# Kernel optimization log

Hardware: AMD Instinct MI355X
Metric: run time of the kernel (lower is better)

The kernel has to match this reference:

```python
import math
import jax, jax.numpy as jnp
import numpy as np

NUM_LEVELS = 3
K = 9          # filter_size
SIGMA = 2.0
OMEGA_X = 0.25
OMEGA_Y = 0.25
C = 64         # channels


def _fan_filter():
    # low-pass Gaussian, shape (C,1,K,K)
    ax = jnp.arange(K, dtype=jnp.float32) - (K - 1) / 2.0
    xx, yy = jnp.meshgrid(ax, ax, indexing='ij')
    lp = jnp.exp(-(xx ** 2 + yy ** 2) / (2.0 * SIGMA ** 2))
    lp = lp / jnp.sum(lp)
    lp = jnp.tile(lp[None, None], (C, 1, 1, 1))
    # high-pass: negate and add delta at center of channel 0 ONLY (faithful to source)
    hp = -lp
    c = K // 2
    hp = hp.at[0, 0, c, c].add(1.0)
    # fan modulation
    cy = jnp.arange(K, dtype=jnp.float32) - K // 2
    cx = jnp.arange(K, dtype=jnp.float32) - K // 2
    y, x = jnp.meshgrid(cy, cx, indexing='ij')
    mod = jnp.cos(2.0 * math.pi * (OMEGA_X * x + OMEGA_Y * y))
    return hp * mod


def _shear_sample(x, s):
    """affine_grid(theta=[[1,s,0],[0,1,0]]) + grid_sample(bilinear, zeros, align_corners=False)."""
    B, Cc, H, W = x.shape
    dt = x.dtype
    # align_corners=False normalized base grid
    xn = (2.0 * jnp.arange(W, dtype=dt) + 1.0) / W - 1.0  # (W,)
    yn = (2.0 * jnp.arange(H, dtype=dt) + 1.0) / H - 1.0  # (H,)
    gx = xn[None, :] + s * yn[:, None]                    # (H,W)
    gy = jnp.broadcast_to(yn[:, None], (H, W))            # (H,W)
    # unnormalize (align_corners=False)
    ix = ((gx + 1.0) * W - 1.0) / 2.0
    iy = ((gy + 1.0) * H - 1.0) / 2.0
    ix0 = jnp.floor(ix); iy0 = jnp.floor(iy)
    ix1 = ix0 + 1.0;     iy1 = iy0 + 1.0
    wx1 = ix - ix0; wx0 = 1.0 - wx1
    wy1 = iy - iy0; wy0 = 1.0 - wy1

    def gather(yi, xi):
        yc = jnp.clip(yi, 0, H - 1).astype(jnp.int32)
        xc = jnp.clip(xi, 0, W - 1).astype(jnp.int32)
        valid = ((yi >= 0) & (yi < H) & (xi >= 0) & (xi < W)).astype(dt)
        return x[:, :, yc, xc] * valid  # (B,C,H,W)

    out = (gather(iy0, ix0) * (wy0 * wx0)
           + gather(iy0, ix1) * (wy0 * wx1)
           + gather(iy1, ix0) * (wy1 * wx0)
           + gather(iy1, ix1) * (wy1 * wx1))
    return out


def _dwconv(x, filt):
    # depthwise cross-correlation, padding K//2 (matches F.conv2d groups=C)
    return jax.lax.conv_general_dilated(
        x, filt, window_strides=(1, 1),
        padding=[(K // 2, K // 2), (K // 2, K // 2)],
        dimension_numbers=('NCHW', 'OIHW', 'NCHW'),
        feature_group_count=C)


def _dfb(x, filt):
    out1 = _dwconv(_shear_sample(x, 1.0), filt)
    out2 = _dwconv(_shear_sample(x, -1.0), filt)
    return out1, out2


def _binary_dfb(x, filt, level):
    if level == 0:
        return [x]
    d1, d2 = _dfb(x, filt)
    return _binary_dfb(d1, filt, level - 1) + _binary_dfb(d2, filt, level - 1)


def setup_inputs() -> dict:
    key = jax.random.key(0)
    x = jax.random.normal(key, (4, C, 256, 256), dtype=jnp.float32)
    filt = _fan_filter()  # buffer (C,1,K,K)
    return {"x": x, "filt": filt}


def reference(x, filt):
    # stack of 2^NUM_LEVELS directional subbands, shape (8, B, C, H, W)
    return jnp.stack(_binary_dfb(x, filt, NUM_LEVELS))
```

## Files before the change

kernel.cpp:

```cpp
#include <hip/hip_runtime.h>
#include <hip/hip_fp16.h>


#define B_ 4
#define C_ 64
#define H_ 256
#define W_ 256
#define TH 32
#define SROWS (TH + 8)
#define SCOLS (W_ + 8)
#define NPB 2048
#define NPB2 1024
#define PSTRIDE 260
#define PPLANE (H_ * PSTRIDE)

struct alignas(4) h8 { unsigned int u[4]; };

struct Factors { float A0, A2, A4, A6, A8, B1, B3, B5, B7, vc[9]; };

static __device__ __forceinline__ Factors mk_factors(const float* __restrict__ filt)
{
    const float* f1 = filt + 81;
    Factors F;
    F.A4 = sqrtf(fmaxf(-f1[4 * 9 + 4], 0.f));
    const float rA4 = 1.f / F.A4;
    F.A0 = -f1[0 * 9 + 4] * rA4;  F.A2 = -f1[2 * 9 + 4] * rA4;
    F.A6 = -f1[6 * 9 + 4] * rA4;  F.A8 = -f1[8 * 9 + 4] * rA4;
    F.B5 = sqrtf(fmaxf(f1[5 * 9 + 5], 0.f));
    const float rB5 = 1.f / F.B5;
    F.B1 = f1[1 * 9 + 5] * rB5;  F.B3 = f1[3 * 9 + 5] * rB5;
    F.B7 = f1[7 * 9 + 5] * rB5;
    F.vc[0] = -F.A0; F.vc[1] = F.B1; F.vc[2] = -F.A2; F.vc[3] = F.B3;
    F.vc[4] = -F.A4; F.vc[5] = F.B5; F.vc[6] = -F.A6; F.vc[7] = F.B7;
    F.vc[8] = -F.A8;
    return F;
}

static __device__ __forceinline__ float4 shear_avg_h(const h8 raw, int d)
{
    union { h8 r; __half2 h2[4]; } U; U.r = raw;
    const bool qhi   = (d & 1) != 0;
    const bool valid = (unsigned)d < 260u;
    const float2 g01 = __half22float2(U.h2[0]);
    const float2 g23 = __half22float2(U.h2[1]);
    const float2 g45 = __half22float2(U.h2[2]);
    const float t0 = qhi ? g01.y : g01.x;
    const float t1 = qhi ? g23.x : g01.y;
    const float t2 = qhi ? g23.y : g23.x;
    const float t3 = qhi ? g45.x : g23.y;
    const float t4 = qhi ? g45.y : g45.x;
    float4 v;
    v.x = valid ? 0.5f * (t0 + t1) : 0.f;
    v.y = valid ? 0.5f * (t1 + t2) : 0.f;
    v.z = valid ? 0.5f * (t2 + t3) : 0.f;
    v.w = valid ? 0.5f * (t3 + t4) : 0.f;
    return v;
}

template<bool DST_H>
static __device__ __forceinline__ void compute_store(
    float (&s_sh)[SROWS][SCOLS], void* __restrict__ dst_, const Factors& F,
    int plane_idx, int c, int h0t, bool first_pad)
{
    const int tid  = threadIdx.x;
    const int rg   = tid >> 6;
    const int lane = tid & 63;
    const int w0   = lane * 4;

    float acc[8][4];
    #pragma unroll
    for (int i = 0; i < 8; ++i)
        #pragma unroll
        for (int j = 0; j < 4; ++j) acc[i][j] = 0.f;

    __builtin_amdgcn_s_setprio(1);
    #pragma unroll
    for (int t = 0; t < 16; ++t) {
        const int rr = rg * 8 + t;
        const float4 sa  = *(const float4*)&s_sh[rr][w0];
        const float4 sb  = *(const float4*)&s_sh[rr][w0 + 4];
        const float4 sc4 = *(const float4*)&s_sh[rr][w0 + 8];
        const float s[12] = {sa.x, sa.y, sa.z, sa.w,
                             sb.x, sb.y, sb.z, sb.w,
                             sc4.x, sc4.y, sc4.z, sc4.w};
        float ha[4], hb[4];
        #pragma unroll
        for (int j = 0; j < 4; ++j) {
            ha[j] = fmaf(F.A8, s[j + 8],
                    fmaf(F.A6, s[j + 6],
                    fmaf(F.A4, s[j + 4],
                    fmaf(F.A2, s[j + 2], F.A0 * s[j]))));
            hb[j] = fmaf(F.B7, s[j + 7],
                    fmaf(F.B5, s[j + 5],
                    fmaf(F.B3, s[j + 3], F.B1 * s[j + 1])));
        }
        #pragma unroll
        for (int i = 0; i < 8; ++i) {
            const int ky = t - i;
            if (ky >= 0 && ky < 9) {
                #pragma unroll
                for (int j = 0; j < 4; ++j) {
                    const float hv = (ky & 1) ? hb[j] : ha[j];
                    acc[i][j] = fmaf(F.vc[ky], hv, acc[i][j]);
                }
            }
        }
    }
    __builtin_amdgcn_s_setprio(0);

    if (c == 0) {
        #pragma unroll
        for (int i = 0; i < 8; ++i) {
            const float4 sv = *(const float4*)&s_sh[rg * 8 + i + 4][w0 + 4];
            acc[i][0] += sv.x; acc[i][1] += sv.y; acc[i][2] += sv.z; acc[i][3] += sv.w;
        }
    }

    if (DST_H) {
        __half* plane = (__half*)dst_ + (size_t)plane_idx * PPLANE;
        if (lane < 8) {
            uint2 z; z.x = 0u; z.y = 0u;
            *(uint2*)(plane + (size_t)(h0t + rg * 8 + lane + 1) * PSTRIDE) = z;
        }
        if (first_pad && tid == 8) {
            uint2 z; z.x = 0u; z.y = 0u;
            *(uint2*)dst_ = z;
        }
        __half* optr = plane + (size_t)(h0t + rg * 8) * PSTRIDE + 4 + (lane * 4);
        #pragma unroll
        for (int i = 0; i < 8; ++i) {
            union { __half2 h2; unsigned int u; } p0, p1;
            p0.h2 = __floats2half2_rn(acc[i][0], acc[i][1]);
            p1.h2 = __floats2half2_rn(acc[i][2], acc[i][3]);
            uint2 pk; pk.x = p0.u; pk.y = p1.u;
            *(uint2*)(optr + (size_t)i * PSTRIDE) = pk;
        }
    } else {
        float* optr = (float*)dst_
            + (((size_t)plane_idx) * H_ + h0t + rg * 8) * (size_t)W_ + w0;
        #pragma unroll
        for (int i = 0; i < 8; ++i) {
            const float4 v = {acc[i][0], acc[i][1], acc[i][2], acc[i][3]};
            *(float4*)(optr + (size_t)i * W_) = v;
        }
    }
}

template<bool DST_H>
__global__ __launch_bounds__(256) void shear_pipe_kernel(
    const void* __restrict__ in_, void* __restrict__ dst_,
    const float* __restrict__ filt, int parity)
{
    __shared__ float s_sh[SROWS][SCOLS];

    const int tid  = threadIdx.x;
    const int bid  = (int)blockIdx.x;
    const int pr   = bid & 3;
    const int c    = (bid >> 2) & 63;
    const int b    = bid >> 8;
    const int h0   = pr * 64;
    const int sign = parity ? -1 : 1;
    const int off  = parity ? 127 : -128;
    const int wave = tid >> 6;
    const int lane = tid & 63;
    const int plane_idx = b * C_ + c;
    const __half* src = (const __half*)in_ + (size_t)plane_idx * PPLANE;

    if (tid < 80) {
        const int r = tid >> 1;
        *(float4*)&s_sh[r][(tid & 1) ? 260 : 0] = make_float4(0.f, 0.f, 0.f, 0.f);
    }

    #pragma unroll
    for (int u = 0; u < 10; ++u) {
        const int r  = wave + u * 4;
        const int hr = h0 + r - 4;
        float4 v = make_float4(0.f, 0.f, 0.f, 0.f);
        if ((unsigned)hr < 256u) {
            const __half* rowh = src + (size_t)hr * PSTRIDE;
            const int d  = off + sign * hr + 4 + lane * 4;
            const int mc = min(max(d & ~1, 0), 258);
            const h8 raw = *(const h8*)(rowh + mc);
            v = shear_avg_h(raw, d);
        }
        *(float4*)&s_sh[r][4 + lane * 4] = v;
    }

    h8 R[10] = {};
    #pragma unroll
    for (int u = 0; u < 10; ++u) {
        const int hr = h0 + 28 + wave + u * 4;
        if ((unsigned)hr < 256u) {
            const __half* rowh = src + (size_t)hr * PSTRIDE;
            const int d  = off + sign * hr + 4 + lane * 4;
            const int mc = min(max(d & ~1, 0), 258);
            R[u] = *(const h8*)(rowh + mc);
        }
    }
    __builtin_amdgcn_sched_barrier(0);

    const Factors F = mk_factors(filt);

    __syncthreads();
    compute_store<DST_H>(s_sh, dst_, F, plane_idx, c, h0, bid == 0);
    __syncthreads();

    #pragma unroll
    for (int u = 0; u < 10; ++u) {
        const int r  = wave + u * 4;
        const int hr = h0 + 28 + r;
        float4 v = make_float4(0.f, 0.f, 0.f, 0.f);
        if ((unsigned)hr < 256u) {
            const int d = off + sign * hr + 4 + lane * 4;
            v = shear_avg_h(R[u], d);
        }
        *(float4*)&s_sh[r][4 + lane * 4] = v;
    }
    __syncthreads();
    compute_store<DST_H>(s_sh, dst_, F, plane_idx, c, h0 + TH, false);
}

__global__ __launch_bounds__(256) void shear_x_kernel(
    const float* __restrict__ in, void* __restrict__ dst_,
    const float* __restrict__ filt, int parity)
{
    __shared__ float s_sh[SROWS][SCOLS];

    const int tid  = threadIdx.x;
    const int bid  = (int)blockIdx.x;
    const int tile = bid & 7;
    const int c    = (bid >> 3) & 63;
    const int b    = bid >> 9;
    const int h0   = tile * TH;
    const int sign = parity ? -1 : 1;
    const int off  = parity ? 127 : -128;
    const int plane_idx = b * C_ + c;

    {
        const int wave = tid >> 6;
        const int lane = tid & 63;

        if (tid < 80) {
            const int r = tid >> 1;
            *(float4*)&s_sh[r][(tid & 1) ? 260 : 0] = make_float4(0.f, 0.f, 0.f, 0.f);
        }

        #pragma unroll
        for (int u = 0; u < 10; ++u) {
            const int r  = wave + u * 4;
            const int hr = h0 + r - 4;
            float4 v = make_float4(0.f, 0.f, 0.f, 0.f);
            if ((unsigned)hr < 256u) {
                const float* row = in + (size_t)plane_idx * (H_ * W_)
                                      + (size_t)hr * W_;
                const int c0 = off + sign * hr + lane * 4;
                float t0 = row[min(max(c0,     0), 255)];
                float t1 = row[min(max(c0 + 1, 0), 255)];
                float t2 = row[min(max(c0 + 2, 0), 255)];
                float t3 = row[min(max(c0 + 3, 0), 255)];
                float t4 = row[min(max(c0 + 4, 0), 255)];
                t0 = ((unsigned)c0       < 256u) ? t0 : 0.f;
                t1 = ((unsigned)(c0 + 1) < 256u) ? t1 : 0.f;
                t2 = ((unsigned)(c0 + 2) < 256u) ? t2 : 0.f;
                t3 = ((unsigned)(c0 + 3) < 256u) ? t3 : 0.f;
                t4 = ((unsigned)(c0 + 4) < 256u) ? t4 : 0.f;
                v.x = 0.5f * (t0 + t1);
                v.y = 0.5f * (t1 + t2);
                v.z = 0.5f * (t2 + t3);
                v.w = 0.5f * (t3 + t4);
            }
            *(float4*)&s_sh[r][4 + lane * 4] = v;
        }
    }

    const Factors F = mk_factors(filt);
    __syncthreads();
    compute_store<true>(s_sh, dst_, F, plane_idx, c, h0, bid == 0);
}

extern "C" void kernel_launch(void* const* d_in, const int* in_sizes, int n_in,
                              void* d_out, int out_size, void* d_ws, size_t ws_size,
                              hipStream_t stream) {
    const float* x    = (const float*)d_in[0];
    const float* filt = (const float*)d_in[1];
    float* out = (float*)d_out;
    void*  wsb = d_ws;
    const size_t N = (size_t)B_ * C_ * H_ * W_;

    float* S[8];
    for (int k = 0; k < 8; ++k) S[k] = out + (size_t)k * N;

    void* Bh  = (void*)S[0];
    void* BAh = (void*)S[2];
    void* BBh = (void*)S[3];
    void* Ah  = (void*)S[1];
    void* AAh = (void*)S[2];
    void* ABh = wsb;

    const dim3 block(256);
    const dim3 gridX(NPB);
    const dim3 gridP(NPB2);

    #define LX(src, dst, par) \
        shear_x_kernel<<<gridX, block, 0, stream>>>(src, dst, filt, par)
    #define LP(DH, src, dst, par) \
        shear_pipe_kernel<DH><<<gridP, block, 0, stream>>>(src, dst, filt, par)

    LX(x, Bh, 1);
    LP(true , Bh,  BAh,  0);
    LP(false, BAh, S[4], 0);
    LP(false, BAh, S[5], 1);
    LP(true , Bh,  BBh,  1);
    LP(false, BBh, S[6], 0);
    LP(false, BBh, S[7], 1);
    LX(x, Ah, 0);
    LP(true , Ah,  AAh,  0);
    LP(true , Ah,  ABh,  1);
    LP(false, AAh, S[0], 0);
    LP(false, AAh, S[1], 1);
    LP(false, ABh, S[2], 0);
    LP(false, ABh, S[3], 1);
    #undef LX
    #undef LP
}
```

Measured before the change: 385.7 us.

## Fuse both shear directions into one pair kernel per input tile

Replaces the single-direction pipe kernel, which covered two 32-row tiles per block, with a pair kernel. Each block handles one 32-row tile and produces both the +1 and -1 shear outputs from the same source rows. This halves the number of launches (12 to 6) and shares input reads across the two directions. The trade-off is that the old overlap of the second tile's loads with the first tile's compute now applies to the second direction instead.

```diff
diff --git a/kernel.cpp b/kernel.cpp
--- a/kernel.cpp
+++ b/kernel.cpp
@@ -10,7 +10,6 @@
 #define SROWS (TH + 8)
 #define SCOLS (W_ + 8)
 #define NPB 2048
-#define NPB2 1024
 #define PSTRIDE 260
 #define PPLANE (H_ * PSTRIDE)
 
@@ -137,7 +136,7 @@
         }
     } else {
         float* optr = (float*)dst_
-            + (((size_t)plane_idx) * H_ + h0t + rg * 8) * (size_t)W_ + w0;
+            + (((size_t)plane_idx) * H_ + h0t + rg * 8) * (size_t)W_ + (lane * 4);
         #pragma unroll
         for (int i = 0; i < 8; ++i) {
             const float4 v = {acc[i][0], acc[i][1], acc[i][2], acc[i][3]};
@@ -147,20 +146,18 @@
 }
 
 template<bool DST_H>
-__global__ __launch_bounds__(256) void shear_pipe_kernel(
-    const void* __restrict__ in_, void* __restrict__ dst_,
-    const float* __restrict__ filt, int parity)
+__global__ __launch_bounds__(256) void shear_pair_kernel(
+    const void* __restrict__ in_, void* __restrict__ dst0_,
+    void* __restrict__ dst1_, const float* __restrict__ filt)
 {
     __shared__ float s_sh[SROWS][SCOLS];
 
     const int tid  = threadIdx.x;
     const int bid  = (int)blockIdx.x;
-    const int pr   = bid & 3;
-    const int c    = (bid >> 2) & 63;
-    const int b    = bid >> 8;
-    const int h0   = pr * 64;
-    const int sign = parity ? -1 : 1;
-    const int off  = parity ? 127 : -128;
+    const int tile = bid & 7;
+    const int c    = (bid >> 3) & 63;
+    const int b    = bid >> 9;
+    const int h0   = tile * TH;
     const int wave = tid >> 6;
     const int lane = tid & 63;
     const int plane_idx = b * C_ + c;
@@ -178,7 +175,7 @@
         float4 v = make_float4(0.f, 0.f, 0.f, 0.f);
         if ((unsigned)hr < 256u) {
             const __half* rowh = src + (size_t)hr * PSTRIDE;
-            const int d  = off + sign * hr + 4 + lane * 4;
+            const int d  = -128 + hr + 4 + lane * 4;
             const int mc = min(max(d & ~1, 0), 258);
             const h8 raw = *(const h8*)(rowh + mc);
             v = shear_avg_h(raw, d);
@@ -189,10 +186,10 @@
     h8 R[10] = {};
     #pragma unroll
     for (int u = 0; u < 10; ++u) {
-        const int hr = h0 + 28 + wave + u * 4;
+        const int hr = h0 + wave + u * 4 - 4;
         if ((unsigned)hr < 256u) {
             const __half* rowh = src + (size_t)hr * PSTRIDE;
-            const int d  = off + sign * hr + 4 + lane * 4;
+            const int d  = 127 - hr + 4 + lane * 4;
             const int mc = min(max(d & ~1, 0), 258);
             R[u] = *(const h8*)(rowh + mc);
         }
@@ -202,22 +199,22 @@
     const Factors F = mk_factors(filt);
 
     __syncthreads();
-    compute_store<DST_H>(s_sh, dst_, F, plane_idx, c, h0, bid == 0);
+    compute_store<DST_H>(s_sh, dst0_, F, plane_idx, c, h0, bid == 0);
     __syncthreads();
 
     #pragma unroll
     for (int u = 0; u < 10; ++u) {
         const int r  = wave + u * 4;
-        const int hr = h0 + 28 + r;
+        const int hr = h0 + r - 4;
         float4 v = make_float4(0.f, 0.f, 0.f, 0.f);
         if ((unsigned)hr < 256u) {
-            const int d = off + sign * hr + 4 + lane * 4;
+            const int d = 127 - hr + 4 + lane * 4;
             v = shear_avg_h(R[u], d);
         }
         *(float4*)&s_sh[r][4 + lane * 4] = v;
     }
     __syncthreads();
-    compute_store<DST_H>(s_sh, dst_, F, plane_idx, c, h0 + TH, false);
+    compute_store<DST_H>(s_sh, dst1_, F, plane_idx, c, h0, bid == 0);
 }
 
 __global__ __launch_bounds__(256) void shear_x_kernel(
@@ -298,28 +295,21 @@
     void* ABh = wsb;
 
     const dim3 block(256);
-    const dim3 gridX(NPB);
-    const dim3 gridP(NPB2);
+    const dim3 grid(NPB);
 
     #define LX(src, dst, par) \
-        shear_x_kernel<<<gridX, block, 0, stream>>>(src, dst, filt, par)
-    #define LP(DH, src, dst, par) \
-        shear_pipe_kernel<DH><<<gridP, block, 0, stream>>>(src, dst, filt, par)
+        shear_x_kernel<<<grid, block, 0, stream>>>(src, dst, filt, par)
+    #define P(DH, src, d0, d1) \
+        shear_pair_kernel<DH><<<grid, block, 0, stream>>>(src, d0, d1, filt)
 
     LX(x, Bh, 1);
-    LP(true , Bh,  BAh,  0);
-    LP(false, BAh, S[4], 0);
-    LP(false, BAh, S[5], 1);
-    LP(true , Bh,  BBh,  1);
-    LP(false, BBh, S[6], 0);
-    LP(false, BBh, S[7], 1);
+    P(true , Bh,  BAh,  BBh );
+    P(false, BAh, S[4], S[5]);
+    P(false, BBh, S[6], S[7]);
     LX(x, Ah, 0);
-    LP(true , Ah,  AAh,  0);
-    LP(true , Ah,  ABh,  1);
-    LP(false, AAh, S[0], 0);
-    LP(false, AAh, S[1], 1);
-    LP(false, ABh, S[2], 0);
-    LP(false, ABh, S[3], 1);
+    P(true , Ah,  AAh,  ABh );
+    P(false, AAh, S[0], S[1]);
+    P(false, ABh, S[2], S[3]);
     #undef LX
-    #undef LP
-}
+    #undef P
+}
```

New measurement: 367.7 us. 1.05x faster.
